# Kernel tuning notes

Hardware: AMD Instinct MI355X
Metric: run time of the kernel (lower is better)

## Reference

```python
import jax, jax.numpy as jnp
import numpy as np

N = 8_000_000   # total nodes across the batch
B = 2048        # number of graphs (segments)
L1 = 1.0 / 50.0


def _bce(p, t):
    # elementwise BCE matching torch.nn.BCELoss: logs clamped at -100
    logp = jnp.clip(jnp.log(p), -100.0)
    log1mp = jnp.clip(jnp.log1p(-p), -100.0)
    return -(t * logp + (1.0 - t) * log1mp)


def setup_inputs() -> dict:
    key = jax.random.key(0)
    k1, k2, k3, k4, k5, k6 = jax.random.split(key, 6)
    y_mus_pred = jax.random.uniform(k1, (N,), dtype=jnp.float32)
    y_mus = jax.random.uniform(k2, (N,), dtype=jnp.float32)
    y_sat_pred = jax.random.uniform(k3, (B,), dtype=jnp.float32)
    y_sat = jax.random.uniform(k4, (B,), dtype=jnp.float32)
    batch = jnp.sort(jax.random.randint(k5, (N,), 0, B, dtype=jnp.int32))
    mask = jax.random.randint(k6, (N,), 0, 2, dtype=jnp.int32)
    return {"y_mus_pred": y_mus_pred, "y_mus": y_mus,
            "y_sat_pred": y_sat_pred, "y_sat": y_sat,
            "batch": batch, "mask": mask}


def reference(y_mus_pred, y_mus, y_sat_pred, y_sat, batch, mask):
    m = mask.astype(y_mus_pred.dtype)
    # per-node BCE on masked predictions (torch: bce_mus(pred*mask, target), reduction='sum' per graph)
    bce = _bce(y_mus_pred * m, y_mus)                      # [N]
    seg_bce = jax.ops.segment_sum(bce, batch, num_segments=B)  # [B]
    seg_cnt = jax.ops.segment_sum(m, batch, num_segments=B)    # [B] = sum(mask) per graph
    per_graph = jnp.where(seg_cnt > 0, seg_bce / jnp.maximum(seg_cnt, 1.0), 0.0)
    total = per_graph.sum()
    # scalar saturation BCE (mean reduction) scaled by L1
    total = total + _bce(y_sat_pred, y_sat).mean() * jnp.asarray(L1, y_sat_pred.dtype)
    return total
```

## Files before the change

kernel.cpp:

```cpp
#include <hip/hip_runtime.h>

#define BLOCK  256
#define WAVES  (BLOCK / 64)
#define WELEM  512
#define BELEM  (WAVES * WELEM)
#define ITERS  2
#define SPAN   (BELEM * ITERS)

__device__ __forceinline__ float bce_elem(float p, float t) {
    float lp  = fmaxf(__logf(p), -100.0f);
    float l1p = fmaxf(__logf(1.0f - p), -100.0f);
    return -__builtin_fmaf(t, lp - l1p, l1p);
}

struct Regs {
    float4 p0, p1, t0, t1;
    int4   s0, s1, m0, m1;
};

__device__ __forceinline__ void load_regs(Regs& r,
    const float* __restrict__ pred, const float* __restrict__ tgt,
    const int* __restrict__ batch, const int* __restrict__ mask,
    long wb, int lane)
{
    const float4* p4 = reinterpret_cast<const float4*>(pred + wb);
    const float4* t4 = reinterpret_cast<const float4*>(tgt + wb);
    const int4*   s4 = reinterpret_cast<const int4*>(batch + wb);
    const int4*   m4 = reinterpret_cast<const int4*>(mask + wb);
    r.p0 = p4[lane]; r.p1 = p4[64 + lane];
    r.t0 = t4[lane]; r.t1 = t4[64 + lane];
    r.s0 = s4[lane]; r.s1 = s4[64 + lane];
    r.m0 = m4[lane]; r.m1 = m4[64 + lane];
}

__device__ __forceinline__ void wave_flush(int s, float b, float c,
    float* __restrict__ seg_bce, float* __restrict__ seg_cnt, int lane)
{
    #pragma unroll
    for (int o = 32; o > 0; o >>= 1) {
        b += __shfl_xor(b, o);
        c += __shfl_xor(c, o);
    }
    if (lane == 0 && s >= 0) {
        atomicAdd(&seg_bce[s], b);
        atomicAdd(&seg_cnt[s], c);
    }
}

__global__ __launch_bounds__(BLOCK) void seg_bce_kernel(
    const float* __restrict__ pred, const float* __restrict__ tgt,
    const int* __restrict__ batch, const int* __restrict__ mask,
    float* __restrict__ seg_bce, float* __restrict__ seg_cnt, int n)
{
    const int wave = threadIdx.x >> 6;
    const int lane = threadIdx.x & 63;
    const long blockBase = (long)blockIdx.x * SPAN;

    int   runSeg = -1;
    float accb = 0.0f, accc = 0.0f;

    Regs r, rn;
    long wb0 = blockBase + (long)wave * WELEM;
    if (wb0 + WELEM <= n) load_regs(r, pred, tgt, batch, mask, wb0, lane);

    #pragma unroll
    for (int i = 0; i < ITERS; ++i) {
        long wb  = blockBase + (long)i * BELEM + (long)wave * WELEM;
        bool vec = (wb + WELEM <= n);

        if (i + 1 < ITERS) {
            long wbn = wb + BELEM;
            if (wbn + WELEM <= n) load_regs(rn, pred, tgt, batch, mask, wbn, lane);
        }

        if (vec) {
            float pv[8] = {r.p0.x, r.p0.y, r.p0.z, r.p0.w, r.p1.x, r.p1.y, r.p1.z, r.p1.w};
            float tv[8] = {r.t0.x, r.t0.y, r.t0.z, r.t0.w, r.t1.x, r.t1.y, r.t1.z, r.t1.w};
            int   sv[8] = {r.s0.x, r.s0.y, r.s0.z, r.s0.w, r.s1.x, r.s1.y, r.s1.z, r.s1.w};
            int   mv[8] = {r.m0.x, r.m0.y, r.m0.z, r.m0.w, r.m1.x, r.m1.y, r.m1.z, r.m1.w};

            int segFirst = __builtin_amdgcn_readfirstlane(r.s0.x);
            int segLast  = __builtin_amdgcn_readfirstlane(__shfl(r.s1.w, 63));

            if (segFirst == segLast) {
                if (runSeg != segFirst) {
                    if (runSeg >= 0) wave_flush(runSeg, accb, accc, seg_bce, seg_cnt, lane);
                    accb = 0.0f; accc = 0.0f; runSeg = segFirst;
                }
                #pragma unroll
                for (int j = 0; j < 8; ++j) {
                    float mf = (float)mv[j];
                    accb += bce_elem(pv[j] * mf, tv[j]);
                    accc += mf;
                }
            } else {
                if (runSeg >= 0) wave_flush(runSeg, accb, accc, seg_bce, seg_cnt, lane);
                accb = 0.0f; accc = 0.0f; runSeg = -1;
                float bv[8], cv[8];
                #pragma unroll
                for (int j = 0; j < 8; ++j) {
                    float mf = (float)mv[j];
                    bv[j] = bce_elem(pv[j] * mf, tv[j]);
                    cv[j] = mf;
                }
                for (int s = segFirst; s <= segLast; ++s) {
                    float pb = 0.0f, pc = 0.0f;
                    #pragma unroll
                    for (int j = 0; j < 8; ++j) {
                        if (sv[j] == s) { pb += bv[j]; pc += cv[j]; }
                    }
                    wave_flush(s, pb, pc, seg_bce, seg_cnt, lane);
                }
            }
        } else if (wb < n) {
            if (runSeg >= 0) wave_flush(runSeg, accb, accc, seg_bce, seg_cnt, lane);
            accb = 0.0f; accc = 0.0f; runSeg = -1;
            int cur = -1; float ab = 0.0f, ac = 0.0f;
            #pragma unroll
            for (int g = 0; g < 2; ++g) {
                for (int e = 0; e < 4; ++e) {
                    long idx = wb + (long)g * 256 + (long)lane * 4 + e;
                    if (idx < n) {
                        int s = batch[idx];
                        if (s != cur) {
                            if (cur >= 0) {
                                atomicAdd(&seg_bce[cur], ab);
                                atomicAdd(&seg_cnt[cur], ac);
                            }
                            cur = s; ab = 0.0f; ac = 0.0f;
                        }
                        float mf = (float)mask[idx];
                        ab += bce_elem(pred[idx] * mf, tgt[idx]);
                        ac += mf;
                    }
                }
            }
            if (cur >= 0) {
                atomicAdd(&seg_bce[cur], ab);
                atomicAdd(&seg_cnt[cur], ac);
            }
        }
        r = rn;
    }

    if (runSeg >= 0) wave_flush(runSeg, accb, accc, seg_bce, seg_cnt, lane);
}

__global__ __launch_bounds__(256) void finalize_kernel(
    const float* __restrict__ seg_bce, const float* __restrict__ seg_cnt,
    const float* __restrict__ sat_pred, const float* __restrict__ sat_tgt,
    float* __restrict__ out, int Bseg)
{
    const float l1_over_b = (1.0f / 50.0f) / (float)Bseg;
    float local = 0.0f;
    for (int i = threadIdx.x; i < Bseg; i += blockDim.x) {
        float c = seg_cnt[i];
        if (c > 0.0f) local += seg_bce[i] / fmaxf(c, 1.0f);
        local += bce_elem(sat_pred[i], sat_tgt[i]) * l1_over_b;
    }
    #pragma unroll
    for (int o = 32; o > 0; o >>= 1) local += __shfl_xor(local, o);
    __shared__ float ws[4];
    if ((threadIdx.x & 63) == 0) ws[threadIdx.x >> 6] = local;
    __syncthreads();
    if (threadIdx.x == 0) out[0] = ws[0] + ws[1] + ws[2] + ws[3];
}

extern "C" void kernel_launch(void* const* d_in, const int* in_sizes, int n_in,
                              void* d_out, int out_size, void* d_ws, size_t ws_size,
                              hipStream_t stream) {
    const float* y_mus_pred = (const float*)d_in[0];
    const float* y_mus      = (const float*)d_in[1];
    const float* y_sat_pred = (const float*)d_in[2];
    const float* y_sat      = (const float*)d_in[3];
    const int*   batch      = (const int*)d_in[4];
    const int*   mask       = (const int*)d_in[5];

    const int n    = in_sizes[0];
    const int Bseg = in_sizes[2];

    float* seg_bce = (float*)d_ws;
    float* seg_cnt = seg_bce + Bseg;

    hipMemsetAsync(d_ws, 0, 2 * (size_t)Bseg * sizeof(float), stream);

    const int nblocks = (n + SPAN - 1) / SPAN;
    seg_bce_kernel<<<nblocks, BLOCK, 0, stream>>>(
        y_mus_pred, y_mus, batch, mask, seg_bce, seg_cnt, n);
    finalize_kernel<<<1, 256, 0, stream>>>(
        seg_bce, seg_cnt, y_sat_pred, y_sat, (float*)d_out, Bseg);
}
```

Measured before the change: 163.6 us.

## Skip batch-array bulk loads via endpoint segment checks and triple-buffered register pipeline

Each wave now reads only the first and last batch index of each 512-element region and loads the full batch vector only when a segment boundary falls inside that region. This cuts roughly a quarter of the DRAM traffic, since the sorted batch array rarely changes within a region. Each wave also processes 4 contiguous regions through a 3-stage register prefetch pipeline with a sched_barrier. The scalar tail is moved to a single wave. Risks are extra scalar loads per region and higher register pressure from three staged buffers.

```diff
diff --git a/kernel.cpp b/kernel.cpp
--- a/kernel.cpp
+++ b/kernel.cpp
@@ -1,36 +1,15 @@
 #include <hip/hip_runtime.h>
 
-#define BLOCK  256
-#define WAVES  (BLOCK / 64)
-#define WELEM  512
-#define BELEM  (WAVES * WELEM)
-#define ITERS  2
-#define SPAN   (BELEM * ITERS)
+#define BLOCK   256
+#define RELEM   512
+#define WREG    4
+#define BREG    (4 * WREG)
+#define STAGES  3
 
 __device__ __forceinline__ float bce_elem(float p, float t) {
     float lp  = fmaxf(__logf(p), -100.0f);
     float l1p = fmaxf(__logf(1.0f - p), -100.0f);
     return -__builtin_fmaf(t, lp - l1p, l1p);
-}
-
-struct Regs {
-    float4 p0, p1, t0, t1;
-    int4   s0, s1, m0, m1;
-};
-
-__device__ __forceinline__ void load_regs(Regs& r,
-    const float* __restrict__ pred, const float* __restrict__ tgt,
-    const int* __restrict__ batch, const int* __restrict__ mask,
-    long wb, int lane)
-{
-    const float4* p4 = reinterpret_cast<const float4*>(pred + wb);
-    const float4* t4 = reinterpret_cast<const float4*>(tgt + wb);
-    const int4*   s4 = reinterpret_cast<const int4*>(batch + wb);
-    const int4*   m4 = reinterpret_cast<const int4*>(mask + wb);
-    r.p0 = p4[lane]; r.p1 = p4[64 + lane];
-    r.t0 = t4[lane]; r.t1 = t4[64 + lane];
-    r.s0 = s4[lane]; r.s1 = s4[64 + lane];
-    r.m0 = m4[lane]; r.m1 = m4[64 + lane];
 }
 
 __device__ __forceinline__ void wave_flush(int s, float b, float c,
@@ -47,6 +26,73 @@
     }
 }
 
+struct Stage {
+    float4 p0, p1, t0, t1;
+    int4   m0, m1;
+    int    sF, sL;
+};
+
+__device__ __forceinline__ void stage_load(Stage& s,
+    const float* __restrict__ pred, const float* __restrict__ tgt,
+    const int* __restrict__ batch, const int* __restrict__ mask,
+    long rb, int lane)
+{
+    s.sF = batch[rb];
+    s.sL = batch[rb + RELEM - 1];
+    const float4* p4 = reinterpret_cast<const float4*>(pred + rb);
+    const float4* t4 = reinterpret_cast<const float4*>(tgt + rb);
+    const int4*   m4 = reinterpret_cast<const int4*>(mask + rb);
+    s.p0 = p4[lane]; s.p1 = p4[64 + lane];
+    s.t0 = t4[lane]; s.t1 = t4[64 + lane];
+    s.m0 = m4[lane]; s.m1 = m4[64 + lane];
+}
+
+__device__ __forceinline__ void consume(const Stage& s, long rb, int lane,
+    int& runSeg, float& accb, float& accc,
+    const int* __restrict__ batch,
+    float* __restrict__ seg_bce, float* __restrict__ seg_cnt)
+{
+    int segF = __builtin_amdgcn_readfirstlane(s.sF);
+    int segL = __builtin_amdgcn_readfirstlane(s.sL);
+
+    float pv[8] = {s.p0.x, s.p0.y, s.p0.z, s.p0.w, s.p1.x, s.p1.y, s.p1.z, s.p1.w};
+    float tv[8] = {s.t0.x, s.t0.y, s.t0.z, s.t0.w, s.t1.x, s.t1.y, s.t1.z, s.t1.w};
+    int   mv[8] = {s.m0.x, s.m0.y, s.m0.z, s.m0.w, s.m1.x, s.m1.y, s.m1.z, s.m1.w};
+
+    if (segF == segL) {
+        if (runSeg != segF) {
+            if (runSeg >= 0) wave_flush(runSeg, accb, accc, seg_bce, seg_cnt, lane);
+            accb = 0.0f; accc = 0.0f; runSeg = segF;
+        }
+        #pragma unroll
+        for (int j = 0; j < 8; ++j) {
+            float mf = (float)mv[j];
+            accb += bce_elem(pv[j] * mf, tv[j]);
+            accc += mf;
+        }
+    } else {
+        if (runSeg >= 0) wave_flush(runSeg, accb, accc, seg_bce, seg_cnt, lane);
+        accb = 0.0f; accc = 0.0f; runSeg = -1;
+        const int4* b4 = reinterpret_cast<const int4*>(batch + rb);
+        int4 s0 = b4[lane], s1 = b4[64 + lane];
+        int sv[8] = {s0.x, s0.y, s0.z, s0.w, s1.x, s1.y, s1.z, s1.w};
+        float bv[8], cv[8];
+        #pragma unroll
+        for (int j = 0; j < 8; ++j) {
+            float mf = (float)mv[j];
+            bv[j] = bce_elem(pv[j] * mf, tv[j]);
+            cv[j] = mf;
+        }
+        for (int g = segF; g <= segL; ++g) {
+            float pb = 0.0f, pc = 0.0f;
+            #pragma unroll
+            for (int j = 0; j < 8; ++j)
+                if (sv[j] == g) { pb += bv[j]; pc += cv[j]; }
+            wave_flush(g, pb, pc, seg_bce, seg_cnt, lane);
+        }
+    }
+}
+
 __global__ __launch_bounds__(BLOCK) void seg_bce_kernel(
     const float* __restrict__ pred, const float* __restrict__ tgt,
     const int* __restrict__ batch, const int* __restrict__ mask,
@@ -54,96 +100,40 @@
 {
     const int wave = threadIdx.x >> 6;
     const int lane = threadIdx.x & 63;
-    const long blockBase = (long)blockIdx.x * SPAN;
+    const int nreg = n >> 9;
+    const long r0  = (long)blockIdx.x * BREG + (long)wave * WREG;
 
     int   runSeg = -1;
     float accb = 0.0f, accc = 0.0f;
-
-    Regs r, rn;
-    long wb0 = blockBase + (long)wave * WELEM;
-    if (wb0 + WELEM <= n) load_regs(r, pred, tgt, batch, mask, wb0, lane);
+    Stage st[STAGES];
 
     #pragma unroll
-    for (int i = 0; i < ITERS; ++i) {
-        long wb  = blockBase + (long)i * BELEM + (long)wave * WELEM;
-        bool vec = (wb + WELEM <= n);
+    for (int k = 0; k < STAGES - 1; ++k)
+        if (r0 + k < nreg)
+            stage_load(st[k], pred, tgt, batch, mask, (r0 + k) * RELEM, lane);
 
-        if (i + 1 < ITERS) {
-            long wbn = wb + BELEM;
-            if (wbn + WELEM <= n) load_regs(rn, pred, tgt, batch, mask, wbn, lane);
+    #pragma unroll
+    for (int i = 0; i < WREG; ++i) {
+        long rp = r0 + i + (STAGES - 1);
+        if (i + (STAGES - 1) < WREG && rp < nreg)
+            stage_load(st[(i + STAGES - 1) % STAGES], pred, tgt, batch, mask,
+                       rp * RELEM, lane);
+        __builtin_amdgcn_sched_barrier(0);
+        long r = r0 + i;
+        if (r < nreg)
+            consume(st[i % STAGES], r * RELEM, lane,
+                    runSeg, accb, accc, batch, seg_bce, seg_cnt);
+    }
+    if (runSeg >= 0) wave_flush(runSeg, accb, accc, seg_bce, seg_cnt, lane);
+
+    if (blockIdx.x == 0 && wave == 0) {
+        for (long idx = (long)nreg * RELEM + lane; idx < n; idx += 64) {
+            float mf = (float)mask[idx];
+            float b  = bce_elem(pred[idx] * mf, tgt[idx]);
+            atomicAdd(&seg_bce[batch[idx]], b);
+            atomicAdd(&seg_cnt[batch[idx]], mf);
         }
-
-        if (vec) {
-            float pv[8] = {r.p0.x, r.p0.y, r.p0.z, r.p0.w, r.p1.x, r.p1.y, r.p1.z, r.p1.w};
-            float tv[8] = {r.t0.x, r.t0.y, r.t0.z, r.t0.w, r.t1.x, r.t1.y, r.t1.z, r.t1.w};
-            int   sv[8] = {r.s0.x, r.s0.y, r.s0.z, r.s0.w, r.s1.x, r.s1.y, r.s1.z, r.s1.w};
-            int   mv[8] = {r.m0.x, r.m0.y, r.m0.z, r.m0.w, r.m1.x, r.m1.y, r.m1.z, r.m1.w};
-
-            int segFirst = __builtin_amdgcn_readfirstlane(r.s0.x);
-            int segLast  = __builtin_amdgcn_readfirstlane(__shfl(r.s1.w, 63));
-
-            if (segFirst == segLast) {
-                if (runSeg != segFirst) {
-                    if (runSeg >= 0) wave_flush(runSeg, accb, accc, seg_bce, seg_cnt, lane);
-                    accb = 0.0f; accc = 0.0f; runSeg = segFirst;
-                }
-                #pragma unroll
-                for (int j = 0; j < 8; ++j) {
-                    float mf = (float)mv[j];
-                    accb += bce_elem(pv[j] * mf, tv[j]);
-                    accc += mf;
-                }
-            } else {
-                if (runSeg >= 0) wave_flush(runSeg, accb, accc, seg_bce, seg_cnt, lane);
-                accb = 0.0f; accc = 0.0f; runSeg = -1;
-                float bv[8], cv[8];
-                #pragma unroll
-                for (int j = 0; j < 8; ++j) {
-                    float mf = (float)mv[j];
-                    bv[j] = bce_elem(pv[j] * mf, tv[j]);
-                    cv[j] = mf;
-                }
-                for (int s = segFirst; s <= segLast; ++s) {
-                    float pb = 0.0f, pc = 0.0f;
-                    #pragma unroll
-                    for (int j = 0; j < 8; ++j) {
-                        if (sv[j] == s) { pb += bv[j]; pc += cv[j]; }
-                    }
-                    wave_flush(s, pb, pc, seg_bce, seg_cnt, lane);
-                }
-            }
-        } else if (wb < n) {
-            if (runSeg >= 0) wave_flush(runSeg, accb, accc, seg_bce, seg_cnt, lane);
-            accb = 0.0f; accc = 0.0f; runSeg = -1;
-            int cur = -1; float ab = 0.0f, ac = 0.0f;
-            #pragma unroll
-            for (int g = 0; g < 2; ++g) {
-                for (int e = 0; e < 4; ++e) {
-                    long idx = wb + (long)g * 256 + (long)lane * 4 + e;
-                    if (idx < n) {
-                        int s = batch[idx];
-                        if (s != cur) {
-                            if (cur >= 0) {
-                                atomicAdd(&seg_bce[cur], ab);
-                                atomicAdd(&seg_cnt[cur], ac);
-                            }
-                            cur = s; ab = 0.0f; ac = 0.0f;
-                        }
-                        float mf = (float)mask[idx];
-                        ab += bce_elem(pred[idx] * mf, tgt[idx]);
-                        ac += mf;
-                    }
-                }
-            }
-            if (cur >= 0) {
-                atomicAdd(&seg_bce[cur], ab);
-                atomicAdd(&seg_cnt[cur], ac);
-            }
-        }
-        r = rn;
     }
-
-    if (runSeg >= 0) wave_flush(runSeg, accb, accc, seg_bce, seg_cnt, lane);
 }
 
 __global__ __launch_bounds__(256) void finalize_kernel(
@@ -184,7 +174,8 @@
 
     hipMemsetAsync(d_ws, 0, 2 * (size_t)Bseg * sizeof(float), stream);
 
-    const int nblocks = (n + SPAN - 1) / SPAN;
+    const int nreg    = n >> 9;
+    const int nblocks = (nreg + BREG - 1) / BREG;
     seg_bce_kernel<<<nblocks, BLOCK, 0, stream>>>(
         y_mus_pred, y_mus, batch, mask, seg_bce, seg_cnt, n);
     finalize_kernel<<<1, 256, 0, stream>>>(
```

After: 164.1 us. About the same (+0.3%).
